# Kernel optimization log

Hardware: AMD Instinct MI355X
Metric: run time of the kernel (lower is better)

## Reference

```python
import jax, jax.numpy as jnp
import numpy as np
from jax import lax

# ---- configuration (matches init_kwargs) ----
B, C_DATA, C_FEAT, H, W = 2, 8, 8, 160, 160
K = 7                      # number of soft nearest neighbors
PS, STRIDE, WIN = 10, 5, 15
FEAT, C_EMB = 64, 8
N1 = (H - PS) // STRIDE + 1   # 31, no padding needed
N2 = (W - PS) // STRIDE + 1   # 31
NEG_INF = -1e9


def _conv3(x, w, b):
    y = lax.conv_general_dilated(x, w, (1, 1), 'SAME',
                                 dimension_numbers=('NCHW', 'OIHW', 'NCHW'))
    return y + b[None, :, None, None]


def _cnn(x, w1, b1, w2, b2, w3, b3):
    # depth-3 DnCNN-style net: conv-relu-conv-relu-conv (bn=False, lastact=linear)
    h = jax.nn.relu(_conv3(x, w1, b1))
    h = jax.nn.relu(_conv3(h, w2, b2))
    return _conv3(h, w3, b3)


def _im2patch(x):
    # x: [b,c,H,W] -> [b,n1,n2,c*PS*PS]; patch flattened channel-major (c,p1,p2)
    ii = jnp.arange(N1)[:, None] * STRIDE + jnp.arange(PS)[None, :]  # [n1,PS]
    jj = jnp.arange(N2)[:, None] * STRIDE + jnp.arange(PS)[None, :]  # [n2,PS]
    p = x[:, :, ii[:, None, :, None], jj[None, :, None, :]]  # [b,c,n1,n2,PS,PS]
    p = jnp.transpose(p, (0, 2, 3, 1, 4, 5))
    return p.reshape(p.shape[0], N1, N2, -1)


def _n3block(x_data, x_faet, ew1, eb1, ew2, eb2, ew3, eb3,
             tw1, tb1, tw2, tb2, tw3, tb3):
    xe = _cnn(x_faet, ew1, eb1, ew2, eb2, ew3, eb3)      # [b,8,H,W] embeddings
    log_temp = _cnn(x_faet, tw1, tb1, tw2, tb2, tw3, tb3)  # [b,1,H,W]

    ye = _im2patch(xe)                        # [b,n1,n2,E]; queries == database
    yp = _im2patch(x_data)                    # [b,n1,n2,F]
    lt = _im2patch(log_temp).mean(-1)         # scalar log-temp per patch
    temp = jnp.exp(lt)[..., None]             # [b,n1,n2,1] (temp_bias = 1)

    S = min(WIN, N1, N2)
    R = S // 2
    base1 = jnp.clip(jnp.arange(N1) - R, 0, N1 - S)   # clamped window top-left
    base2 = jnp.clip(jnp.arange(N2) - R, 0, N2 - S)
    offs = jnp.stack(jnp.meshgrid(jnp.arange(S), jnp.arange(S), indexing='ij'),
                     axis=-1).reshape(-1, 2)          # [S*S,2]
    i1, i2 = jnp.arange(N1), jnp.arange(N2)
    yn = jnp.sum(ye * ye, axis=-1)            # [b,n1,n2] squared norms

    @jax.checkpoint
    def dist_step(carry, off):
        j1 = base1 + off[0]
        j2 = base2 + off[1]
        xs = ye[:, j1][:, :, j2]              # [b,n1,n2,E] candidate embedding
        xn = yn[:, j1][:, :, j2]
        dot = jnp.einsum('bije,bije->bij', ye, xs)
        d = yn + xn - 2.0 * dot               # squared euclidean distance
        self_m = (j1 == i1)[:, None] & (j2 == i2)[None, :]
        return carry, (d, self_m)

    _, (D, selfm) = lax.scan(dist_step, None, offs)
    D = jnp.moveaxis(D, 0, -1)                # [b,n1,n2,O], O=S*S
    selfm = jnp.moveaxis(selfm, 0, -1)        # [n1,n2,O]

    logits = -D / temp
    logits = jnp.where(selfm, NEG_INF, logits)   # exclude_self

    # continuous deterministic top-k (N3Net): w_j = softmax(a); a += log(1 - w_j)
    ws = []
    for _ in range(K):
        wgt = jax.nn.softmax(logits, axis=-1)
        ws.append(wgt)
        logits = logits + jnp.log1p(-jnp.minimum(wgt, 1.0 - 1e-6))
    Wk = jnp.stack(ws, axis=-1)               # [b,n1,n2,O,K]

    @jax.checkpoint
    def agg_step(z, args):
        off, wk = args                        # wk: [b,n1,n2,K]
        j1 = base1 + off[0]
        j2 = base2 + off[1]
        ys = yp[:, j1][:, :, j2]              # [b,n1,n2,F]
        return z + wk[..., :, None] * ys[..., None, :], None

    z0 = jnp.zeros(yp.shape[:3] + (K, yp.shape[-1]), yp.dtype)
    z, _ = lax.scan(agg_step, z0, (offs, jnp.moveaxis(Wk, 3, 0)))
    z = z - yp[..., None, :]                  # residue=True
    out_p = jnp.concatenate([yp[..., None, :], z], axis=3)  # [b,n1,n2,K+1,F]

    # fold patch volumes back to image, averaging overlaps
    b = out_p.shape[0]
    C = (K + 1) * C_DATA
    out_p = out_p.reshape(b, N1, N2, K + 1, C_DATA, PS, PS)
    out_p = jnp.transpose(out_p, (0, 3, 4, 1, 2, 5, 6)).reshape(b, C, N1, N2, PS, PS)
    rows = jnp.arange(N1)[:, None] * STRIDE + jnp.arange(PS)[None, :]
    cols = jnp.arange(N2)[:, None] * STRIDE + jnp.arange(PS)[None, :]
    lin = (rows[:, None, :, None] * W + cols[None, :, None, :]).reshape(-1)
    vals = out_p.reshape(b, C, -1)
    img = jnp.zeros((b, C, H * W), out_p.dtype).at[:, :, lin].add(vals)
    cnt = jnp.zeros((H * W,), out_p.dtype).at[lin].add(1.0)
    return (img / cnt).reshape(b, C, H, W)


def setup_inputs() -> dict:
    key = jax.random.key(0)
    ks = jax.random.split(key, 8)
    f32 = jnp.float32
    wn = lambda k, s: jax.random.normal(k, s, f32) * 0.05
    return dict(
        x_data=jax.random.normal(ks[0], (B, C_DATA, H, W), f32),
        x_faet=jax.random.normal(ks[1], (B, C_FEAT, H, W), f32),
        ew1=wn(ks[2], (FEAT, C_FEAT, 3, 3)), eb1=jnp.zeros((FEAT,), f32),
        ew2=wn(ks[3], (FEAT, FEAT, 3, 3)), eb2=jnp.zeros((FEAT,), f32),
        ew3=wn(ks[4], (C_EMB, FEAT, 3, 3)), eb3=jnp.zeros((C_EMB,), f32),
        tw1=wn(ks[5], (FEAT, C_FEAT, 3, 3)), tb1=jnp.zeros((FEAT,), f32),
        tw2=wn(ks[6], (FEAT, FEAT, 3, 3)), tb2=jnp.zeros((FEAT,), f32),
        tw3=wn(ks[7], (1, FEAT, 3, 3)), tb3=jnp.zeros((1,), f32),
    )


def reference(x_data, x_faet, ew1, eb1, ew2, eb2, ew3, eb3,
              tw1, tb1, tw2, tb2, tw3, tb3):
    return _n3block(x_data, x_faet, ew1, eb1, ew2, eb2, ew3, eb3,
                    tw1, tb1, tw2, tb2, tw3, tb3)
```

## Files before the change

kernel.cpp:

```cpp
#include <hip/hip_runtime.h>
#include <math.h>

#define BN 2
#define HH 160
#define WW 160
#define CDATA 8
#define PS 10
#define STR 5
#define N1 31
#define N2 31
#define NSITE (N1*N2)
#define SITES (BN*NSITE)
#define SWIN 15
#define NOFF 225
#define KK 7
#define EDIM 800
#define NPIX 25600
#define LP 40
#define KP 480
#define COLP 992
#define GP 34
#define KSPLIT 5

typedef __attribute__((ext_vector_type(8))) short s8v;
typedef __attribute__((ext_vector_type(8))) unsigned short u8v;
typedef __attribute__((ext_vector_type(4))) float f4v;

__device__ __forceinline__ unsigned short f2bf(float f) {
    unsigned u = __float_as_uint(f);
    return (unsigned short)((u + 0x7FFFu + ((u >> 16) & 1u)) >> 16);
}
__device__ __forceinline__ float bf2f(unsigned short h) {
    return __uint_as_float(((unsigned)h) << 16);
}

__device__ __forceinline__ float block_sum(float v, float* sred) {
    #pragma unroll
    for (int o = 32; o; o >>= 1) v += __shfl_xor(v, o);
    __syncthreads();
    if ((threadIdx.x & 63) == 0) sred[threadIdx.x >> 6] = v;
    __syncthreads();
    return sred[0] + sred[1] + sred[2] + sred[3];
}

__global__ __launch_bounds__(256) void prep_k(const float* __restrict__ xd,
                                              const float* __restrict__ ew2,
                                              const float* __restrict__ tw2,
                                              const float* __restrict__ ew1,
                                              const float* __restrict__ tw1,
                                              unsigned short* __restrict__ ypT,
                                              unsigned short* __restrict__ wp,
                                              unsigned short* __restrict__ wp1) {
    int blk = blockIdx.x;
    int t = threadIdx.x;
    if (blk < 1600) {
        int b = blk / 800, e = blk % 800;
        int cd = e & 7, pp = e >> 3;
        int pi = pp / 10, pj = pp % 10;
        const float* src = xd + ((size_t)(b * 8 + cd) * HH + pi) * WW + pj;
        unsigned short* dst = ypT + (size_t)blk * COLP;
        for (int it = 0; it < 4; ++it) {
            int col = it * 256 + t;
            if (col < COLP) {
                int j1 = col >> 5, j2 = col & 31;
                unsigned short v = 0;
                if (j2 < 31) v = f2bf(src[(j1 * 5) * WW + j2 * 5]);
                dst[col] = v;
            }
        }
    } else if (blk < 1888) {
        int idx = (blk - 1600) * 256 + t;
        int which = idx / (64 * 576); int r = idx % (64 * 576);
        int n = r / 576, k = r % 576;
        int p = k / 64, c = k % 64;
        const float* w = which ? tw2 : ew2;
        wp[idx] = f2bf(w[(n * 64 + c) * 9 + p]);
    } else {
        int idx = (blk - 1888) * 256 + t;
        if (idx < 128 * 96) {
            int n = idx / 96, k = idx % 96;
            int tap = k >> 3, c = k & 7;
            unsigned short v = 0;
            if (tap < 9) {
                const float* w = (n < 64) ? ew1 : tw1;
                v = f2bf(w[((n & 63) * 8 + c) * 9 + tap]);
            }
            wp1[idx] = v;
        }
    }
}

__global__ __launch_bounds__(256) void conv1_mfma_k(const float* __restrict__ xf,
                                                    const unsigned short* __restrict__ wp1,
                                                    const float* __restrict__ eb1,
                                                    const float* __restrict__ tb1,
                                                    unsigned short* __restrict__ h1) {
    __shared__ unsigned short Al[128 * LP];
    __shared__ unsigned short Bl[64 * LP];
    const int t = threadIdx.x;
    const int m0 = blockIdx.x * 64;
    const int wv = t >> 6, lane = t & 63;
    f4v acc[2][4];
    #pragma unroll
    for (int fj = 0; fj < 2; ++fj)
        #pragma unroll
        for (int fi = 0; fi < 4; ++fi) { f4v z = {0.f,0.f,0.f,0.f}; acc[fj][fi] = z; }
    const int mp = m0 + (t >> 2);
    const int b = mp / NPIX, rp = mp % NPIX;
    const int py = rp / WW, px = rp % WW;
    for (int ks = 0; ks < 3; ++ks) {
        int tap = ks * 4 + (t & 3);
        int dy = tap / 3 - 1, dx = tap % 3 - 1;
        int yy = py + dy, xx = px + dx;
        bool ok = (tap < 9) && yy >= 0 && yy < HH && xx >= 0 && xx < WW;
        u8v bv;
        #pragma unroll
        for (int c = 0; c < 8; ++c)
            bv[c] = ok ? f2bf(xf[((size_t)(b * 8 + c)) * NPIX + yy * WW + xx]) : 0;
        __syncthreads();
        *(u8v*)(Bl + (t >> 2) * LP + (t & 3) * 8) = bv;
        #pragma unroll
        for (int it = 0; it < 2; ++it) {
            int idx = t + it * 256;
            int row = idx >> 2, seg = idx & 3;
            *(u8v*)(Al + row * LP + seg * 8) = *(const u8v*)(wp1 + row * 96 + ks * 32 + seg * 8);
        }
        __syncthreads();
        s8v af[2], bf[4];
        #pragma unroll
        for (int fj = 0; fj < 2; ++fj)
            af[fj] = *(const s8v*)((const short*)Al + (wv * 32 + fj * 16 + (lane & 15)) * LP + (lane >> 4) * 8);
        #pragma unroll
        for (int fi = 0; fi < 4; ++fi)
            bf[fi] = *(const s8v*)((const short*)Bl + (fi * 16 + (lane & 15)) * LP + (lane >> 4) * 8);
        #pragma unroll
        for (int fj = 0; fj < 2; ++fj)
            #pragma unroll
            for (int fi = 0; fi < 4; ++fi)
                acc[fj][fi] = __builtin_amdgcn_mfma_f32_16x16x32_bf16(af[fj], bf[fi], acc[fj][fi], 0, 0, 0);
    }
    #pragma unroll
    for (int fj = 0; fj < 2; ++fj) {
        int nb = wv * 32 + fj * 16 + (lane >> 4) * 4;
        float bias4[4];
        #pragma unroll
        for (int c = 0; c < 4; ++c) {
            int n = nb + c;
            bias4[c] = (n < 64) ? eb1[n] : tb1[n - 64];
        }
        #pragma unroll
        for (int fi = 0; fi < 4; ++fi) {
            int mm = m0 + fi * 16 + (lane & 15);
            ushort4 o;
            o.x = f2bf(fmaxf(acc[fj][fi][0] + bias4[0], 0.f));
            o.y = f2bf(fmaxf(acc[fj][fi][1] + bias4[1], 0.f));
            o.z = f2bf(fmaxf(acc[fj][fi][2] + bias4[2], 0.f));
            o.w = f2bf(fmaxf(acc[fj][fi][3] + bias4[3], 0.f));
            *(ushort4*)(h1 + (size_t)mm * 128 + nb) = o;
        }
    }
}

__global__ __launch_bounds__(256) void conv2_mfma_k(const unsigned short* __restrict__ h1,
                                                    const unsigned short* __restrict__ wp,
                                                    const float* __restrict__ eb2,
                                                    const float* __restrict__ tb2,
                                                    unsigned short* __restrict__ h2) {
    __shared__ unsigned short Al[64 * LP];
    __shared__ unsigned short Bl[64 * LP];
    const int t = threadIdx.x;
    const int which = blockIdx.y;
    const int m0 = blockIdx.x * 64;
    const int wv = t >> 6, lane = t & 63;
    const int n0w = (wv >> 1) * 32, m0w = (wv & 1) * 32;
    f4v a00 = {0.f,0.f,0.f,0.f}, a01 = a00, a10 = a00, a11 = a00;
    const unsigned short* wb = wp + (size_t)which * 64 * 576;
    const int sm = t >> 2, sq = (t & 3) * 8;
    const int mp = m0 + sm;
    const int b = mp / NPIX, rp = mp % NPIX;
    const int py = rp / WW, px = rp % WW;
    for (int step = 0; step < 18; ++step) {
        const int p = step >> 1, ch = (step & 1) * 32;
        const int dy = p / 3 - 1, dx = p % 3 - 1;
        s8v av = *(const s8v*)(wb + sm * 576 + p * 64 + ch + sq);
        s8v bv;
        #pragma unroll
        for (int j = 0; j < 8; j++) bv[j] = 0;
        int yy = py + dy, xx = px + dx;
        if (yy >= 0 && yy < HH && xx >= 0 && xx < WW)
            bv = *(const s8v*)((const short*)h1 + ((size_t)b * NPIX + yy * WW + xx) * 128 + which * 64 + ch + sq);
        __syncthreads();
        *(s8v*)((short*)Al + sm * LP + sq) = av;
        *(s8v*)((short*)Bl + sm * LP + sq) = bv;
        __syncthreads();
        s8v af0 = *(const s8v*)((const short*)Al + (n0w      + (lane & 15)) * LP + (lane >> 4) * 8);
        s8v af1 = *(const s8v*)((const short*)Al + (n0w + 16 + (lane & 15)) * LP + (lane >> 4) * 8);
        s8v bf0 = *(const s8v*)((const short*)Bl + (m0w      + (lane & 15)) * LP + (lane >> 4) * 8);
        s8v bf1 = *(const s8v*)((const short*)Bl + (m0w + 16 + (lane & 15)) * LP + (lane >> 4) * 8);
        a00 = __builtin_amdgcn_mfma_f32_16x16x32_bf16(af0, bf0, a00, 0, 0, 0);
        a01 = __builtin_amdgcn_mfma_f32_16x16x32_bf16(af0, bf1, a01, 0, 0, 0);
        a10 = __builtin_amdgcn_mfma_f32_16x16x32_bf16(af1, bf0, a10, 0, 0, 0);
        a11 = __builtin_amdgcn_mfma_f32_16x16x32_bf16(af1, bf1, a11, 0, 0, 0);
    }
    const float* bias = which ? tb2 : eb2;
    #pragma unroll
    for (int fj = 0; fj < 2; ++fj) {
        int nb = n0w + fj * 16 + (lane >> 4) * 4;
        f4v bv4 = *(const f4v*)(bias + nb);
        #pragma unroll
        for (int fi = 0; fi < 2; ++fi) {
            f4v ac = fj ? (fi ? a11 : a10) : (fi ? a01 : a00);
            int mm = m0 + m0w + fi * 16 + (lane & 15);
            ushort4 o;
            o.x = f2bf(fmaxf(ac[0] + bv4[0], 0.f));
            o.y = f2bf(fmaxf(ac[1] + bv4[1], 0.f));
            o.z = f2bf(fmaxf(ac[2] + bv4[2], 0.f));
            o.w = f2bf(fmaxf(ac[3] + bv4[3], 0.f));
            *(ushort4*)(h2 + ((size_t)which * 51200 + mm) * 64 + nb) = o;
        }
    }
}

__global__ __launch_bounds__(256) void conv3_k(const unsigned short* __restrict__ h2,
                                               const float* __restrict__ ew3,
                                               const float* __restrict__ eb3,
                                               const float* __restrict__ tw3,
                                               const float* __restrict__ tb3,
                                               float* __restrict__ xe,
                                               float* __restrict__ ltm) {
    int x = blockIdx.x * 16 + threadIdx.x;
    int y = blockIdx.y * 16 + threadIdx.y;
    int z = blockIdx.z; int b = z >> 1, which = z & 1;
    const unsigned short* h2b = h2 + ((size_t)which * 51200 + b * NPIX) * 64;
    if (which == 0) {
        float acc[8];
        #pragma unroll
        for (int u = 0; u < 8; u++) acc[u] = eb3[u];
        #pragma unroll
        for (int pos = 0; pos < 9; ++pos) {
            int yy = y + pos / 3 - 1, xx = x + pos % 3 - 1;
            if (yy < 0 || yy >= HH || xx < 0 || xx >= WW) continue;
            const unsigned short* row = h2b + ((size_t)yy * WW + xx) * 64;
            for (int cq = 0; cq < 8; ++cq) {
                u8v v = *(const u8v*)(row + cq * 8);
                #pragma unroll
                for (int j = 0; j < 8; ++j) {
                    float f = bf2f(v[j]);
                    int c = cq * 8 + j;
                    #pragma unroll
                    for (int u = 0; u < 8; u++)
                        acc[u] = fmaf(f, ew3[(u * 64 + c) * 9 + pos], acc[u]);
                }
            }
        }
        float* dst = xe + ((size_t)b * NPIX + y * WW + x) * 8;
        #pragma unroll
        for (int u = 0; u < 8; u++) dst[u] = acc[u];
    } else {
        float acc = tb3[0];
        #pragma unroll
        for (int pos = 0; pos < 9; ++pos) {
            int yy = y + pos / 3 - 1, xx = x + pos % 3 - 1;
            if (yy < 0 || yy >= HH || xx < 0 || xx >= WW) continue;
            const unsigned short* row = h2b + ((size_t)yy * WW + xx) * 64;
            for (int cq = 0; cq < 8; ++cq) {
                u8v v = *(const u8v*)(row + cq * 8);
                #pragma unroll
                for (int j = 0; j < 8; ++j)
                    acc = fmaf(bf2f(v[j]), tw3[(cq * 8 + j) * 9 + pos], acc);
            }
        }
        ltm[b * NPIX + y * WW + x] = acc;
    }
}

__global__ __launch_bounds__(256) void im2patch_k(const float* __restrict__ xe,
                                                  const float* __restrict__ ltm,
                                                  unsigned short* __restrict__ yeH,
                                                  unsigned short* __restrict__ yeL,
                                                  float* __restrict__ yn,
                                                  float* __restrict__ tempv) {
    __shared__ float sred[4];
    int site = blockIdx.x;
    int b = site / NSITE; int ij = site % NSITE;
    int i1 = ij / N2, i2 = ij % N2;
    int t = threadIdx.x;
    const float* xeb = xe + (size_t)b * NPIX * 8;
    float ssq = 0.f;
    for (int e = t; e < EDIM; e += 256) {
        int rr = e / 80, rem = e % 80;
        float v = xeb[((size_t)(i1 * STR + rr) * WW + i2 * STR) * 8 + rem];
        unsigned short h = f2bf(v);
        float lo = v - bf2f(h);
        yeH[(size_t)site * EDIM + e] = h;
        yeL[(size_t)site * EDIM + e] = f2bf(lo);
        ssq += v * v;
    }
    float tot = block_sum(ssq, sred);
    if (t == 0) yn[site] = tot;
    float sl = 0.f;
    if (t < 100) {
        int rr = t / 10, q = t % 10;
        sl = ltm[(size_t)b * NPIX + (i1 * STR + rr) * WW + (i2 * STR + q)];
    }
    float slt = block_sum(sl, sred);
    if (t == 0) tempv[site] = expf(slt * (1.f / 100.f));
}

__global__ __launch_bounds__(256) void gram_mfma_k(const unsigned short* __restrict__ yeH,
                                                   const unsigned short* __restrict__ yeL,
                                                   float* __restrict__ dotsC) {
    __shared__ unsigned short AsH[32 * GP], AsL[32 * GP];
    __shared__ unsigned short BsH[256 * GP], BsL[256 * GP];
    int blk = blockIdx.x;
    int kc = blk % KSPLIT; int r = blk / KSPLIT;
    int nh = r & 1; r >>= 1;
    int b = r / N1, i1 = r % N1;
    int b1 = min(max(i1 - 7, 0), 16);
    int t = threadIdx.x;
    int wv = t >> 6, lane = t & 63;
    f4v acc[2][4];
    #pragma unroll
    for (int mt = 0; mt < 2; ++mt)
        #pragma unroll
        for (int nt = 0; nt < 4; ++nt) { f4v z = {0.f,0.f,0.f,0.f}; acc[mt][nt] = z; }
    const size_t abase = (size_t)((b * N1 + i1) * N2) * EDIM;
    for (int ks = kc * 5; ks < kc * 5 + 5; ++ks) {
        __syncthreads();
        {
            int idx = t & 127;
            int row = idx >> 2, seg = idx & 3;
            u8v v;
            #pragma unroll
            for (int u = 0; u < 8; ++u) v[u] = 0;
            if (row < 31)
                v = *(const u8v*)((t < 128 ? yeH : yeL) + abase + (size_t)row * EDIM + ks * 32 + seg * 8);
            *(u8v*)((t < 128 ? AsH : AsL) + row * GP + seg * 8) = v;
        }
        #pragma unroll
        for (int rep = 0; rep < 8; ++rep) {
            int idx = t + rep * 256;
            int isH = idx < 1024;
            int id2 = idx & 1023;
            int row = id2 >> 2, seg = id2 & 3;
            int dj = nh * 8 + (row >> 5), j2 = row & 31;
            u8v v;
            #pragma unroll
            for (int u = 0; u < 8; ++u) v[u] = 0;
            if (dj < 15 && j2 < 31) {
                size_t site = (size_t)((b * N1 + b1 + dj) * N2 + j2);
                v = *(const u8v*)((isH ? yeH : yeL) + site * EDIM + ks * 32 + seg * 8);
            }
            *(u8v*)((isH ? BsH : BsL) + row * GP + seg * 8) = v;
        }
        __syncthreads();
        s8v afH[2], afL[2], bfH[4], bfL[4];
        #pragma unroll
        for (int mt = 0; mt < 2; ++mt) {
            int ar = mt * 16 + (lane & 15);
            afH[mt] = *(const s8v*)((const short*)AsH + ar * GP + (lane >> 4) * 8);
            afL[mt] = *(const s8v*)((const short*)AsL + ar * GP + (lane >> 4) * 8);
        }
        #pragma unroll
        for (int nt = 0; nt < 4; ++nt) {
            int br = wv * 64 + nt * 16 + (lane & 15);
            bfH[nt] = *(const s8v*)((const short*)BsH + br * GP + (lane >> 4) * 8);
            bfL[nt] = *(const s8v*)((const short*)BsL + br * GP + (lane >> 4) * 8);
        }
        #pragma unroll
        for (int mt = 0; mt < 2; ++mt)
            #pragma unroll
            for (int nt = 0; nt < 4; ++nt) {
                acc[mt][nt] = __builtin_amdgcn_mfma_f32_16x16x32_bf16(afH[mt], bfH[nt], acc[mt][nt], 0, 0, 0);
                acc[mt][nt] = __builtin_amdgcn_mfma_f32_16x16x32_bf16(afH[mt], bfL[nt], acc[mt][nt], 0, 0, 0);
                acc[mt][nt] = __builtin_amdgcn_mfma_f32_16x16x32_bf16(afL[mt], bfH[nt], acc[mt][nt], 0, 0, 0);
            }
    }
    float* dk = dotsC + (size_t)kc * SITES * NOFF;
    #pragma unroll
    for (int mt = 0; mt < 2; ++mt) {
        int i2b = mt * 16 + (lane >> 4) * 4;
        #pragma unroll
        for (int nt = 0; nt < 4; ++nt) {
            int n = wv * 64 + nt * 16 + (lane & 15);
            int dj = nh * 8 + (n >> 5), j2 = n & 31;
            if (dj >= 15 || j2 >= 31) continue;
            #pragma unroll
            for (int c = 0; c < 4; ++c) {
                int i2 = i2b + c;
                if (i2 >= 31) continue;
                int b2 = min(max(i2 - 7, 0), 16);
                int dc = j2 - b2;
                if (dc < 0 || dc >= SWIN) continue;
                size_t site = (size_t)((b * N1 + i1) * N2 + i2);
                dk[site * NOFF + dj * SWIN + dc] = acc[mt][nt][c];
            }
        }
    }
}

__global__ __launch_bounds__(256) void softmax_k(const float* __restrict__ dotsC,
                                                 const float* __restrict__ yn,
                                                 const float* __restrict__ tempv,
                                                 float* __restrict__ wkout) {
    int wid = blockIdx.x * 4 + (threadIdx.x >> 6);
    if (wid >= SITES) return;
    int lane = threadIdx.x & 63;
    int b = wid / NSITE; int ij = wid % NSITE;
    int i1 = ij / N2, i2 = ij % N2;
    int b1 = min(max(i1 - 7, 0), 16);
    int b2 = min(max(i2 - 7, 0), 16);
    float yns = yn[wid];
    float tvi = 1.f / tempv[wid];
    float lg[4];
    #pragma unroll
    for (int r = 0; r < 4; ++r) {
        int t = lane + 64 * r;
        lg[r] = -1e9f;
        if (t < NOFF) {
            float dot = 0.f;
            #pragma unroll
            for (int kc = 0; kc < KSPLIT; ++kc)
                dot += dotsC[((size_t)kc * SITES + wid) * NOFF + t];
            int dj = t / SWIN, dc = t % SWIN;
            int j1 = b1 + dj, j2 = b2 + dc;
            float xn = yn[(b * N1 + j1) * N2 + j2];
            float d = yns + xn - 2.f * dot;
            lg[r] = -d * tvi;
            if (j1 == i1 && j2 == i2) lg[r] = -1e9f;
        }
    }
    float* wkr = wkout + (size_t)wid * (KK * NOFF);
    for (int k = 0; k < KK; ++k) {
        float m = fmaxf(fmaxf(lg[0], lg[1]), fmaxf(lg[2], lg[3]));
        #pragma unroll
        for (int o = 32; o; o >>= 1) m = fmaxf(m, __shfl_xor(m, o));
        float ex[4]; float s = 0.f;
        #pragma unroll
        for (int r = 0; r < 4; ++r) { ex[r] = expf(lg[r] - m); s += ex[r]; }
        #pragma unroll
        for (int o = 32; o; o >>= 1) s += __shfl_xor(s, o);
        float inv = 1.f / s;
        #pragma unroll
        for (int r = 0; r < 4; ++r) {
            float wgt = ex[r] * inv;
            int t = lane + 64 * r;
            if (t < NOFF) wkr[k * NOFF + t] = wgt;
            lg[r] += log1pf(-fminf(wgt, 1.f - 1e-6f));
        }
    }
}

__global__ __launch_bounds__(256) void abuild_k(const float* __restrict__ wk,
                                                unsigned short* __restrict__ Aglob) {
    int idx = blockIdx.x * 256 + threadIdx.x;
    if (idx >= 2 * 31 * 256 * 60) return;
    int kc8 = (idx % 60) * 8;
    int m   = (idx / 60) % 256;
    int i1  = (idx / (60 * 256)) % 31;
    int b   = idx / (60 * 256 * 31);
    int dj = kc8 >> 5, j2base = kc8 & 31;
    int pglob = m >> 4, slot = m & 15;
    int s = (slot >= 7) ? 1 : 0;
    int i2 = 2 * pglob + s;
    int k = slot - 7 * s;
    bool valid = (slot < 14) && (i2 <= 30);
    u8v o;
    #pragma unroll
    for (int u = 0; u < 8; ++u) o[u] = 0;
    if (valid) {
        int b2 = min(max(i2 - 7, 0), 16);
        int site = (b * N1 + i1) * N2 + i2;
        const float* wr = wk + (size_t)site * (KK * NOFF) + k * NOFF + dj * SWIN - b2;
        #pragma unroll
        for (int u = 0; u < 8; ++u) {
            int j2 = j2base + u;
            int dc = j2 - b2;
            if (j2 < 31 && dc >= 0 && dc < SWIN) o[u] = f2bf(wr[j2]);
        }
    }
    *(u8v*)(Aglob + (size_t)idx * 8) = o;
}

__global__ __launch_bounds__(256) void agg_gemm_k(const unsigned short* __restrict__ Aglob,
                                                  const unsigned short* __restrict__ ypT,
                                                  unsigned short* __restrict__ zbuf) {
    __shared__ unsigned short As[128 * 40];
    __shared__ unsigned short Bs[160 * 40];
    int blk = blockIdx.x;
    int b = blk / 310; int r = blk % 310;
    int i1 = r / 10; int r2 = r % 10;
    int mh = r2 / 5, nc = r2 % 5;
    int b1 = min(max(i1 - 7, 0), 16);
    int t = threadIdx.x;
    int wv = t >> 6, lane = t & 63;
    int wm = (wv & 1) * 64, we = (wv >> 1) * 80;
    const unsigned short* Ab = Aglob + ((size_t)(b * N1 + i1) * 256 + mh * 128) * KP;
    const unsigned short* Bb = ypT + ((size_t)b * 800 + nc * 160) * COLP + b1 * 32;
    f4v accr[4][5];
    #pragma unroll
    for (int mt = 0; mt < 4; ++mt)
        #pragma unroll
        for (int et = 0; et < 5; ++et) { f4v z = {0.f,0.f,0.f,0.f}; accr[mt][et] = z; }
    for (int ks = 0; ks < 15; ++ks) {
        __syncthreads();
        #pragma unroll
        for (int it = 0; it < 2; ++it) {
            int idx = t + it * 256;
            int row = idx >> 2, seg = idx & 3;
            *(u8v*)(As + row * 40 + seg * 8) = *(const u8v*)(Ab + (size_t)row * KP + ks * 32 + seg * 8);
        }
        #pragma unroll
        for (int it = 0; it < 3; ++it) {
            int idx = t + it * 256;
            if (idx < 640) {
                int row = idx >> 2, seg = idx & 3;
                *(u8v*)(Bs + row * 40 + seg * 8) = *(const u8v*)(Bb + (size_t)row * COLP + ks * 32 + seg * 8);
            }
        }
        __syncthreads();
        s8v af[4], bf[5];
        #pragma unroll
        for (int mt = 0; mt < 4; ++mt)
            af[mt] = *(const s8v*)((const short*)As + (wm + mt * 16 + (lane & 15)) * 40 + (lane >> 4) * 8);
        #pragma unroll
        for (int et = 0; et < 5; ++et)
            bf[et] = *(const s8v*)((const short*)Bs + (we + et * 16 + (lane & 15)) * 40 + (lane >> 4) * 8);
        #pragma unroll
        for (int mt = 0; mt < 4; ++mt)
            #pragma unroll
            for (int et = 0; et < 5; ++et)
                accr[mt][et] = __builtin_amdgcn_mfma_f32_16x16x32_bf16(af[mt], bf[et], accr[mt][et], 0, 0, 0);
    }
    unsigned short* zb = zbuf + ((size_t)(b * N1 + i1) * 256 + mh * 128) * 800 + nc * 160;
    #pragma unroll
    for (int mt = 0; mt < 4; ++mt) {
        int mrow = wm + mt * 16 + (lane >> 4) * 4;
        #pragma unroll
        for (int et = 0; et < 5; ++et) {
            int ecol = we + et * 16 + (lane & 15);
            #pragma unroll
            for (int c = 0; c < 4; ++c)
                zb[(size_t)(mrow + c) * 800 + ecol] = f2bf(accr[mt][et][c]);
        }
    }
}

__global__ __launch_bounds__(256) void finalize_k(const unsigned short* __restrict__ zbuf,
                                                  const float* __restrict__ xd,
                                                  float* __restrict__ out) {
    int pid = blockIdx.x * 256 + threadIdx.x;
    if (pid >= BN * NPIX) return;
    int b = pid / NPIX, pix = pid % NPIX;
    int h = pix / WW, w_ = pix % WW;
    int lo1 = max(0, (h - 5) / 5),  hi1 = min(30, h / 5);
    int lo2 = max(0, (w_ - 5) / 5), hi2 = min(30, w_ / 5);
    float cntinv = 1.f / (float)((hi1 - lo1 + 1) * (hi2 - lo2 + 1));
    float xv[8];
    #pragma unroll
    for (int cd = 0; cd < 8; ++cd) {
        xv[cd] = xd[((size_t)(b * 8 + cd)) * NPIX + pix];
        out[((size_t)(b * 64 + cd)) * NPIX + pix] = xv[cd];
    }
    for (int k = 0; k < KK; ++k) {
        float s[8];
        #pragma unroll
        for (int cd = 0; cd < 8; ++cd) s[cd] = 0.f;
        for (int i1 = lo1; i1 <= hi1; ++i1) {
            int pi = h - 5 * i1;
            for (int i2 = lo2; i2 <= hi2; ++i2) {
                int pj = w_ - 5 * i2;
                int m = 16 * (i2 >> 1) + k + 7 * (i2 & 1);
                const unsigned short* zp = zbuf + ((size_t)(b * N1 + i1) * 256 + m) * 800 + (pi * 10 + pj) * 8;
                u8v zv = *(const u8v*)zp;
                #pragma unroll
                for (int cd = 0; cd < 8; ++cd) s[cd] += bf2f(zv[cd]);
            }
        }
        #pragma unroll
        for (int cd = 0; cd < 8; ++cd)
            out[((size_t)(b * 64 + (k + 1) * 8 + cd)) * NPIX + pix] = s[cd] * cntinv - xv[cd];
    }
}

extern "C" void kernel_launch(void* const* d_in, const int* in_sizes, int n_in,
                              void* d_out, int out_size, void* d_ws, size_t ws_size,
                              hipStream_t stream) {
    (void)in_sizes; (void)n_in; (void)out_size; (void)ws_size;
    const float* x_data = (const float*)d_in[0];
    const float* x_faet = (const float*)d_in[1];
    const float* ew1 = (const float*)d_in[2];  const float* eb1 = (const float*)d_in[3];
    const float* ew2 = (const float*)d_in[4];  const float* eb2 = (const float*)d_in[5];
    const float* ew3 = (const float*)d_in[6];  const float* eb3 = (const float*)d_in[7];
    const float* tw1 = (const float*)d_in[8];  const float* tb1 = (const float*)d_in[9];
    const float* tw2 = (const float*)d_in[10]; const float* tb2 = (const float*)d_in[11];
    const float* tw3 = (const float*)d_in[12]; const float* tb3 = (const float*)d_in[13];
    float* out = (float*)d_out;

    char* base = (char*)d_ws;
    unsigned short* h1 = (unsigned short*)(base);
    unsigned short* h2 = (unsigned short*)(base + 13107200);
    unsigned short* wp1 = (unsigned short*)(base + 13107200);
    unsigned short* wp = (unsigned short*)(base + 26214400);
    float* yn    = (float*)(base + 26361856);
    float* tempv = (float*)(base + 26370048);
    unsigned short* ypT = (unsigned short*)(base + 26378240);
    float* xe    = (float*)(base + 29552640);
    float* ltm   = (float*)(base + 31191040);
    unsigned short* yeH = (unsigned short*)(base + 31395840);
    unsigned short* yeL = (unsigned short*)(base + 34471040);
    unsigned short* Aglob = (unsigned short*)(base + 29552640);
    float* dotsC = (float*)h2;
    float* wkbuf = (float*)h1;
    unsigned short* zbuf = (unsigned short*)base;

    prep_k<<<1936, 256, 0, stream>>>(x_data, ew2, tw2, ew1, tw1, ypT, wp, wp1);
    conv1_mfma_k<<<800, 256, 0, stream>>>(x_faet, wp1, eb1, tb1, h1);
    conv2_mfma_k<<<dim3(800, 2), 256, 0, stream>>>(h1, wp, eb2, tb2, h2);
    conv3_k<<<dim3(10, 10, 4), dim3(16, 16), 0, stream>>>(h2, ew3, eb3, tw3, tb3, xe, ltm);

    im2patch_k<<<BN * NSITE, 256, 0, stream>>>(xe, ltm, yeH, yeL, yn, tempv);
    gram_mfma_k<<<BN * N1 * 2 * KSPLIT, 256, 0, stream>>>(yeH, yeL, dotsC);
    softmax_k<<<(SITES + 3) / 4, 256, 0, stream>>>(dotsC, yn, tempv, wkbuf);

    abuild_k<<<(2 * 31 * 256 * 60) / 256, 256, 0, stream>>>(wkbuf, Aglob);
    agg_gemm_k<<<BN * 310, 256, 0, stream>>>(Aglob, ypT, zbuf);
    finalize_k<<<(BN * NPIX + 255) / 256, 256, 0, stream>>>(zbuf, x_data, out);
}
```

Before: 194.6 us.

## Move conv3 to MFMA with split-bf16 weights and widen conv2 tiles

```diff
diff --git a/kernel.cpp b/kernel.cpp
--- a/kernel.cpp
+++ b/kernel.cpp
@@ -48,9 +48,12 @@
                                               const float* __restrict__ tw2,
                                               const float* __restrict__ ew1,
                                               const float* __restrict__ tw1,
+                                              const float* __restrict__ ew3,
+                                              const float* __restrict__ tw3,
                                               unsigned short* __restrict__ ypT,
                                               unsigned short* __restrict__ wp,
-                                              unsigned short* __restrict__ wp1) {
+                                              unsigned short* __restrict__ wp1,
+                                              unsigned short* __restrict__ wp3) {
     int blk = blockIdx.x;
     int t = threadIdx.x;
     if (blk < 1600) {
@@ -75,7 +78,7 @@
         int p = k / 64, c = k % 64;
         const float* w = which ? tw2 : ew2;
         wp[idx] = f2bf(w[(n * 64 + c) * 9 + p]);
-    } else {
+    } else if (blk < 1936) {
         int idx = (blk - 1888) * 256 + t;
         if (idx < 128 * 96) {
             int n = idx / 96, k = idx % 96;
@@ -86,6 +89,19 @@
                 v = f2bf(w[((n & 63) * 8 + c) * 9 + tap]);
             }
             wp1[idx] = v;
+        }
+    } else {
+        int idx = (blk - 1936) * 256 + t;
+        if (idx < 2 * 16 * 576) {
+            int which = idx / (16 * 576); int r = idx % (16 * 576);
+            int n = r / 576, k = r % 576;
+            int tap = k / 64, c = k % 64;
+            float w = 0.f; bool lo = false;
+            if (which == 0) { w = ew3[((n & 7) * 64 + c) * 9 + tap]; lo = (n >= 8); }
+            else if (n < 2) { w = tw3[c * 9 + tap]; lo = (n == 1); }
+            unsigned short hi = f2bf(w);
+            wp3[idx] = lo ? f2bf(w - bf2f(hi)) : hi;
+            if (which == 1 && n >= 2) wp3[idx] = 0;
         }
     }
 }
@@ -167,110 +183,140 @@
                                                     const float* __restrict__ tb2,
                                                     unsigned short* __restrict__ h2) {
     __shared__ unsigned short Al[64 * LP];
-    __shared__ unsigned short Bl[64 * LP];
+    __shared__ unsigned short Bl[128 * LP];
     const int t = threadIdx.x;
     const int which = blockIdx.y;
-    const int m0 = blockIdx.x * 64;
+    const int m0 = blockIdx.x * 128;
     const int wv = t >> 6, lane = t & 63;
-    const int n0w = (wv >> 1) * 32, m0w = (wv & 1) * 32;
-    f4v a00 = {0.f,0.f,0.f,0.f}, a01 = a00, a10 = a00, a11 = a00;
+    f4v acc[4][2];
+    #pragma unroll
+    for (int nf = 0; nf < 4; ++nf)
+        #pragma unroll
+        for (int mf = 0; mf < 2; ++mf) { f4v z = {0.f,0.f,0.f,0.f}; acc[nf][mf] = z; }
     const unsigned short* wb = wp + (size_t)which * 64 * 576;
     const int sm = t >> 2, sq = (t & 3) * 8;
-    const int mp = m0 + sm;
-    const int b = mp / NPIX, rp = mp % NPIX;
-    const int py = rp / WW, px = rp % WW;
+    const int mp0 = m0 + sm;
+    const int b0 = mp0 / NPIX, rp0 = mp0 % NPIX;
+    const int py0 = rp0 / WW, px0 = rp0 % WW;
+    const int mp1 = m0 + 64 + sm;
+    const int b1_ = mp1 / NPIX, rp1 = mp1 % NPIX;
+    const int py1 = rp1 / WW, px1 = rp1 % WW;
     for (int step = 0; step < 18; ++step) {
         const int p = step >> 1, ch = (step & 1) * 32;
         const int dy = p / 3 - 1, dx = p % 3 - 1;
         s8v av = *(const s8v*)(wb + sm * 576 + p * 64 + ch + sq);
-        s8v bv;
-        #pragma unroll
-        for (int j = 0; j < 8; j++) bv[j] = 0;
-        int yy = py + dy, xx = px + dx;
+        s8v bv0, bv1;
+        #pragma unroll
+        for (int j = 0; j < 8; j++) { bv0[j] = 0; bv1[j] = 0; }
+        int yy = py0 + dy, xx = px0 + dx;
         if (yy >= 0 && yy < HH && xx >= 0 && xx < WW)
-            bv = *(const s8v*)((const short*)h1 + ((size_t)b * NPIX + yy * WW + xx) * 128 + which * 64 + ch + sq);
+            bv0 = *(const s8v*)((const short*)h1 + ((size_t)b0 * NPIX + yy * WW + xx) * 128 + which * 64 + ch + sq);
+        yy = py1 + dy; xx = px1 + dx;
+        if (yy >= 0 && yy < HH && xx >= 0 && xx < WW)
+            bv1 = *(const s8v*)((const short*)h1 + ((size_t)b1_ * NPIX + yy * WW + xx) * 128 + which * 64 + ch + sq);
         __syncthreads();
         *(s8v*)((short*)Al + sm * LP + sq) = av;
-        *(s8v*)((short*)Bl + sm * LP + sq) = bv;
-        __syncthreads();
-        s8v af0 = *(const s8v*)((const short*)Al + (n0w      + (lane & 15)) * LP + (lane >> 4) * 8);
-        s8v af1 = *(const s8v*)((const short*)Al + (n0w + 16 + (lane & 15)) * LP + (lane >> 4) * 8);
-        s8v bf0 = *(const s8v*)((const short*)Bl + (m0w      + (lane & 15)) * LP + (lane >> 4) * 8);
-        s8v bf1 = *(const s8v*)((const short*)Bl + (m0w + 16 + (lane & 15)) * LP + (lane >> 4) * 8);
-        a00 = __builtin_amdgcn_mfma_f32_16x16x32_bf16(af0, bf0, a00, 0, 0, 0);
-        a01 = __builtin_amdgcn_mfma_f32_16x16x32_bf16(af0, bf1, a01, 0, 0, 0);
-        a10 = __builtin_amdgcn_mfma_f32_16x16x32_bf16(af1, bf0, a10, 0, 0, 0);
-        a11 = __builtin_amdgcn_mfma_f32_16x16x32_bf16(af1, bf1, a11, 0, 0, 0);
+        *(s8v*)((short*)Bl + sm * LP + sq) = bv0;
+        *(s8v*)((short*)Bl + (64 + sm) * LP + sq) = bv1;
+        __syncthreads();
+        s8v af[4], bf[2];
+        #pragma unroll
+        for (int nf = 0; nf < 4; ++nf)
+            af[nf] = *(const s8v*)((const short*)Al + (nf * 16 + (lane & 15)) * LP + (lane >> 4) * 8);
+        #pragma unroll
+        for (int mf = 0; mf < 2; ++mf)
+            bf[mf] = *(const s8v*)((const short*)Bl + (wv * 32 + mf * 16 + (lane & 15)) * LP + (lane >> 4) * 8);
+        #pragma unroll
+        for (int nf = 0; nf < 4; ++nf)
+            #pragma unroll
+            for (int mf = 0; mf < 2; ++mf)
+                acc[nf][mf] = __builtin_amdgcn_mfma_f32_16x16x32_bf16(af[nf], bf[mf], acc[nf][mf], 0, 0, 0);
     }
     const float* bias = which ? tb2 : eb2;
     #pragma unroll
-    for (int fj = 0; fj < 2; ++fj) {
-        int nb = n0w + fj * 16 + (lane >> 4) * 4;
+    for (int nf = 0; nf < 4; ++nf) {
+        int nb = nf * 16 + (lane >> 4) * 4;
         f4v bv4 = *(const f4v*)(bias + nb);
         #pragma unroll
-        for (int fi = 0; fi < 2; ++fi) {
-            f4v ac = fj ? (fi ? a11 : a10) : (fi ? a01 : a00);
-            int mm = m0 + m0w + fi * 16 + (lane & 15);
+        for (int mf = 0; mf < 2; ++mf) {
+            int mm = m0 + wv * 32 + mf * 16 + (lane & 15);
             ushort4 o;
-            o.x = f2bf(fmaxf(ac[0] + bv4[0], 0.f));
-            o.y = f2bf(fmaxf(ac[1] + bv4[1], 0.f));
-            o.z = f2bf(fmaxf(ac[2] + bv4[2], 0.f));
-            o.w = f2bf(fmaxf(ac[3] + bv4[3], 0.f));
+            o.x = f2bf(fmaxf(acc[nf][mf][0] + bv4[0], 0.f));
+            o.y = f2bf(fmaxf(acc[nf][mf][1] + bv4[1], 0.f));
+            o.z = f2bf(fmaxf(acc[nf][mf][2] + bv4[2], 0.f));
+            o.w = f2bf(fmaxf(acc[nf][mf][3] + bv4[3], 0.f));
             *(ushort4*)(h2 + ((size_t)which * 51200 + mm) * 64 + nb) = o;
         }
     }
 }
 
-__global__ __launch_bounds__(256) void conv3_k(const unsigned short* __restrict__ h2,
-                                               const float* __restrict__ ew3,
-                                               const float* __restrict__ eb3,
-                                               const float* __restrict__ tw3,
-                                               const float* __restrict__ tb3,
-                                               float* __restrict__ xe,
-                                               float* __restrict__ ltm) {
-    int x = blockIdx.x * 16 + threadIdx.x;
-    int y = blockIdx.y * 16 + threadIdx.y;
-    int z = blockIdx.z; int b = z >> 1, which = z & 1;
-    const unsigned short* h2b = h2 + ((size_t)which * 51200 + b * NPIX) * 64;
-    if (which == 0) {
-        float acc[8];
-        #pragma unroll
-        for (int u = 0; u < 8; u++) acc[u] = eb3[u];
-        #pragma unroll
-        for (int pos = 0; pos < 9; ++pos) {
-            int yy = y + pos / 3 - 1, xx = x + pos % 3 - 1;
-            if (yy < 0 || yy >= HH || xx < 0 || xx >= WW) continue;
-            const unsigned short* row = h2b + ((size_t)yy * WW + xx) * 64;
-            for (int cq = 0; cq < 8; ++cq) {
-                u8v v = *(const u8v*)(row + cq * 8);
+__global__ __launch_bounds__(256) void conv3_mfma_k(const unsigned short* __restrict__ h2,
+                                                    const unsigned short* __restrict__ wp3,
+                                                    const float* __restrict__ eb3,
+                                                    const float* __restrict__ tb3,
+                                                    float* __restrict__ xe,
+                                                    float* __restrict__ ltm) {
+    __shared__ unsigned short Al[16 * LP];
+    __shared__ unsigned short Bl[128 * LP];
+    const int t = threadIdx.x;
+    const int which = blockIdx.y;
+    const int m0 = blockIdx.x * 128;
+    const int wv = t >> 6, lane = t & 63;
+    f4v acc[2];
+    { f4v z = {0.f,0.f,0.f,0.f}; acc[0] = z; acc[1] = z; }
+    const unsigned short* wb = wp3 + (size_t)which * 16 * 576;
+    const int sm = t >> 2, sq = (t & 3) * 8;
+    const int mp0 = m0 + sm;
+    const int b0 = mp0 / NPIX, rp0 = mp0 % NPIX;
+    const int py0 = rp0 / WW, px0 = rp0 % WW;
+    const int mp1 = m0 + 64 + sm;
+    const int b1_ = mp1 / NPIX, rp1 = mp1 % NPIX;
+    const int py1 = rp1 / WW, px1 = rp1 % WW;
+    for (int step = 0; step < 18; ++step) {
+        const int p = step >> 1, ch = (step & 1) * 32;
+        const int dy = p / 3 - 1, dx = p % 3 - 1;
+        s8v av;
+        if (t < 64) av = *(const s8v*)(wb + (t >> 2) * 576 + p * 64 + ch + (t & 3) * 8);
+        s8v bv0, bv1;
+        #pragma unroll
+        for (int j = 0; j < 8; j++) { bv0[j] = 0; bv1[j] = 0; }
+        int yy = py0 + dy, xx = px0 + dx;
+        if (yy >= 0 && yy < HH && xx >= 0 && xx < WW)
+            bv0 = *(const s8v*)((const short*)h2 + ((size_t)which * 51200 + (size_t)b0 * NPIX + yy * WW + xx) * 64 + ch + sq);
+        yy = py1 + dy; xx = px1 + dx;
+        if (yy >= 0 && yy < HH && xx >= 0 && xx < WW)
+            bv1 = *(const s8v*)((const short*)h2 + ((size_t)which * 51200 + (size_t)b1_ * NPIX + yy * WW + xx) * 64 + ch + sq);
+        __syncthreads();
+        if (t < 64) *(s8v*)((short*)Al + (t >> 2) * LP + (t & 3) * 8) = av;
+        *(s8v*)((short*)Bl + sm * LP + sq) = bv0;
+        *(s8v*)((short*)Bl + (64 + sm) * LP + sq) = bv1;
+        __syncthreads();
+        s8v af = *(const s8v*)((const short*)Al + (lane & 15) * LP + (lane >> 4) * 8);
+        #pragma unroll
+        for (int mf = 0; mf < 2; ++mf) {
+            s8v bf = *(const s8v*)((const short*)Bl + (wv * 32 + mf * 16 + (lane & 15)) * LP + (lane >> 4) * 8);
+            acc[mf] = __builtin_amdgcn_mfma_f32_16x16x32_bf16(af, bf, acc[mf], 0, 0, 0);
+        }
+    }
+    #pragma unroll
+    for (int mf = 0; mf < 2; ++mf) {
+        int mm = m0 + wv * 32 + mf * 16 + (lane & 15);
+        if (which == 0) {
+            f4v hilo;
+            #pragma unroll
+            for (int c = 0; c < 4; ++c)
+                hilo[c] = acc[mf][c] + __shfl_xor(acc[mf][c], 32);
+            if (lane < 32) {
+                int nb = (lane >> 4) * 4;
+                f4v o;
                 #pragma unroll
-                for (int j = 0; j < 8; ++j) {
-                    float f = bf2f(v[j]);
-                    int c = cq * 8 + j;
-                    #pragma unroll
-                    for (int u = 0; u < 8; u++)
-                        acc[u] = fmaf(f, ew3[(u * 64 + c) * 9 + pos], acc[u]);
-                }
-            }
-        }
-        float* dst = xe + ((size_t)b * NPIX + y * WW + x) * 8;
-        #pragma unroll
-        for (int u = 0; u < 8; u++) dst[u] = acc[u];
-    } else {
-        float acc = tb3[0];
-        #pragma unroll
-        for (int pos = 0; pos < 9; ++pos) {
-            int yy = y + pos / 3 - 1, xx = x + pos % 3 - 1;
-            if (yy < 0 || yy >= HH || xx < 0 || xx >= WW) continue;
-            const unsigned short* row = h2b + ((size_t)yy * WW + xx) * 64;
-            for (int cq = 0; cq < 8; ++cq) {
-                u8v v = *(const u8v*)(row + cq * 8);
-                #pragma unroll
-                for (int j = 0; j < 8; ++j)
-                    acc = fmaf(bf2f(v[j]), tw3[(cq * 8 + j) * 9 + pos], acc);
-            }
-        }
-        ltm[b * NPIX + y * WW + x] = acc;
+                for (int c = 0; c < 4; ++c) o[c] = hilo[c] + eb3[nb + c];
+                *(f4v*)(xe + (size_t)mm * 8 + nb) = o;
+            }
+        } else {
+            if ((lane >> 4) == 0)
+                ltm[mm] = acc[mf][0] + acc[mf][1] + tb3[0];
+        }
     }
 }
 
@@ -609,15 +655,16 @@
     float* ltm   = (float*)(base + 31191040);
     unsigned short* yeH = (unsigned short*)(base + 31395840);
     unsigned short* yeL = (unsigned short*)(base + 34471040);
+    unsigned short* wp3 = (unsigned short*)(base + 37546240);
     unsigned short* Aglob = (unsigned short*)(base + 29552640);
     float* dotsC = (float*)h2;
     float* wkbuf = (float*)h1;
     unsigned short* zbuf = (unsigned short*)base;
 
-    prep_k<<<1936, 256, 0, stream>>>(x_data, ew2, tw2, ew1, tw1, ypT, wp, wp1);
+    prep_k<<<2008, 256, 0, stream>>>(x_data, ew2, tw2, ew1, tw1, ew3, tw3, ypT, wp, wp1, wp3);
     conv1_mfma_k<<<800, 256, 0, stream>>>(x_faet, wp1, eb1, tb1, h1);
-    conv2_mfma_k<<<dim3(800, 2), 256, 0, stream>>>(h1, wp, eb2, tb2, h2);
-    conv3_k<<<dim3(10, 10, 4), dim3(16, 16), 0, stream>>>(h2, ew3, eb3, tw3, tb3, xe, ltm);
+    conv2_mfma_k<<<dim3(400, 2), 256, 0, stream>>>(h1, wp, eb2, tb2, h2);
+    conv3_mfma_k<<<dim3(400, 2), 256, 0, stream>>>(h2, wp3, eb3, tb3, xe, ltm);
 
     im2patch_k<<<BN * NSITE, 256, 0, stream>>>(xe, ltm, yeH, yeL, yn, tempv);
     gram_mfma_k<<<BN * N1 * 2 * KSPLIT, 256, 0, stream>>>(yeH, yeL, dotsC);
```

Result: faster. 175.5 us (-9.8%).
